# Kernel optimization log

Measured on AMD Instinct MI355X. Metric: run time of the kernel, lower is better.

## Reference

```python
import jax, jax.numpy as jnp
import numpy as np

D_MODEL = 1024
D_FFN = 4096
H = 16
D_HEAD = D_MODEL // H
B, L = 2, 2048
EPS = 1e-6


def layer_norm(x, a, b):
    # Matches torch: std is unbiased (ddof=1), and divides by (std + eps)
    mean = jnp.mean(x, axis=-1, keepdims=True)
    var = jnp.sum((x - mean) ** 2, axis=-1, keepdims=True) / (x.shape[-1] - 1)
    std = jnp.sqrt(var)
    return (x - mean) / (std + EPS) * a + b


def setup_inputs() -> dict:
    key = jax.random.key(0)
    ks = jax.random.split(key, 10)
    s = 0.02
    x = jax.random.normal(ks[0], (B, L, D_MODEL), dtype=jnp.float32)
    mask = jnp.tril(jnp.ones((L, L), dtype=jnp.int32))[None, None]  # causal [1,1,L,L]
    return {
        "x": x,
        "mask": mask,
        "Wqkv": jax.random.normal(ks[1], (D_MODEL, 3 * D_MODEL), jnp.float32) * s,
        "bqkv": jnp.zeros((3 * D_MODEL,), jnp.float32),
        "Wo": jax.random.normal(ks[2], (D_MODEL, D_MODEL), jnp.float32) * s,
        "bo": jnp.zeros((D_MODEL,), jnp.float32),
        "W1": jax.random.normal(ks[3], (D_MODEL, D_FFN), jnp.float32) * s,
        "b1": jnp.zeros((D_FFN,), jnp.float32),
        "W2": jax.random.normal(ks[4], (D_FFN, D_MODEL), jnp.float32) * s,
        "b2": jnp.zeros((D_MODEL,), jnp.float32),
        "ln1_a": jnp.ones((D_MODEL,), jnp.float32),
        "ln1_b": jnp.zeros((D_MODEL,), jnp.float32),
        "ln2_a": jnp.ones((D_MODEL,), jnp.float32),
        "ln2_b": jnp.zeros((D_MODEL,), jnp.float32),
    }


def reference(x, mask, Wqkv, bqkv, Wo, bo, W1, b1, W2, b2, ln1_a, ln1_b, ln2_a, ln2_b):
    b, l, d = x.shape
    # --- attention sublayer ---
    qkv = x @ Wqkv + bqkv                                   # [b, l, 3*d]
    qkv = qkv.reshape(b, l, 3, H, D_HEAD)                   # '(three h d)' ordering
    q, k, v = qkv[:, :, 0], qkv[:, :, 1], qkv[:, :, 2]      # each [b, l, h, dh]
    scores = jnp.einsum('bqhd,bkhd->bhqk', q, k) / jnp.sqrt(
        jnp.asarray(D_HEAD, x.dtype))                        # [b, h, lq, lk]
    scores = jnp.where(mask == 0, -jnp.inf, scores)
    p = jax.nn.softmax(scores, axis=-1)
    attn = jnp.einsum('bhqk,bkhd->bqhd', p, v).reshape(b, l, d)
    attn_out = attn @ Wo + bo
    x = layer_norm(x + attn_out, ln1_a, ln1_b)
    # --- MLP sublayer ---
    h = jax.nn.relu(x @ W1 + b1)
    mlp_out = h @ W2 + b2
    return layer_norm(x + mlp_out, ln2_a, ln2_b)
```

## Files before the change

### kernel.cpp

```cpp
#include <hip/hip_runtime.h>

#define D_MODEL 1024
#define D_FFN   4096
#define NH      16
#define DH      64
#define BB      2
#define LL      2048
#define MROWS   (BB * LL)

typedef unsigned short u16;
typedef unsigned int   u32;
typedef short bf16x8 __attribute__((ext_vector_type(8)));
typedef float f32x4  __attribute__((ext_vector_type(4)));

__device__ __forceinline__ float bf2f(u16 u) {
    union { u32 i; float f; } v;
    v.i = ((u32)u) << 16;
    return v.f;
}
__device__ __forceinline__ u16 f2bf(float f) {
    union { float f; u32 i; } v;
    v.f = f;
    u32 x = v.i;
    x += 0x7fffu + ((x >> 16) & 1u);
    return (u16)(x >> 16);
}
__device__ __forceinline__ float wave_sum(float v) {
    #pragma unroll
    for (int o = 32; o > 0; o >>= 1) v += __shfl_xor(v, o, 64);
    return v;
}
__device__ __forceinline__ u32 pack_bf_trunc(float a, float b) {
    return __builtin_amdgcn_perm(__float_as_uint(b), __float_as_uint(a),
                                 0x07060302u);
}

typedef const __attribute__((address_space(1))) u32 gu32;
typedef __attribute__((address_space(3))) u32 lu32;
__device__ __forceinline__ void gload_lds16(const void* g, void* l) {
    __builtin_amdgcn_global_load_lds((gu32*)g, (lu32*)l, 16, 0, 0);
}

__global__ __launch_bounds__(256) void cvt_kernel(
    const float* __restrict__ in, u16* __restrict__ out, int n)
{
    int i = (blockIdx.x * 256 + threadIdx.x) * 8;
    if (i >= n) return;
    float4 a = *(const float4*)(in + i);
    float4 b = *(const float4*)(in + i + 4);
    u16 o[8] = {f2bf(a.x), f2bf(a.y), f2bf(a.z), f2bf(a.w),
                f2bf(b.x), f2bf(b.y), f2bf(b.z), f2bf(b.w)};
    *(uint4*)(out + i) = *(const uint4*)o;
}

__global__ __launch_bounds__(256) void wt_kernel(
    const float* __restrict__ W, u16* __restrict__ Wt, int K, int N)
{
    __shared__ float tile[64][65];
    const int tid = threadIdx.x;
    const int n0 = blockIdx.x * 64;
    const int k0 = blockIdx.y * 64;

    int kr = tid >> 4;
    int nc = (tid & 15) * 4;
    #pragma unroll
    for (int p = 0; p < 4; ++p) {
        float4 v = *(const float4*)&W[(size_t)(k0 + kr + p * 16) * N + n0 + nc];
        tile[kr + p * 16][nc + 0] = v.x;
        tile[kr + p * 16][nc + 1] = v.y;
        tile[kr + p * 16][nc + 2] = v.z;
        tile[kr + p * 16][nc + 3] = v.w;
    }
    __syncthreads();

    int nr = tid >> 2;
    int kc = (tid & 3) * 16;
    u16 o[16];
    #pragma unroll
    for (int j = 0; j < 16; ++j) o[j] = f2bf(tile[kc + j][nr]);
    u16* dst = &Wt[(size_t)(n0 + nr) * K + k0 + kc];
    *(uint4*)dst       = *(const uint4*)&o[0];
    *(uint4*)(dst + 8) = *(const uint4*)&o[8];
}

template <int EPI, int RF32, int OF32>
__global__ __launch_bounds__(256) void gemm_bt_kernel(
    const u16* __restrict__ A, const u16* __restrict__ Bt,
    const float* __restrict__ bias, const void* __restrict__ resv,
    void* __restrict__ out0v, u16* __restrict__ out1, u16* __restrict__ out2,
    int M, int N, int K)
{
    __shared__ u16 sA[128 * 64];
    __shared__ u16 sB[128 * 64];

    const int tid  = threadIdx.x;
    const int lane = tid & 63;
    const int wave = tid >> 6;
    const int wm   = (wave & 1) * 64;
    const int wn   = (wave >> 1) * 64;
    const int quad = lane >> 4;
    const int l16  = lane & 15;

    const int nb  = gridDim.x;
    const int mb  = gridDim.y;
    const int f   = blockIdx.y * nb + blockIdx.x;
    const int xcd = f & 7;
    const int idx = f >> 3;
    const int rn  = nb >> 1;
    const int rm  = mb >> 2;
    const int n0  = ((xcd & 1) * rn + (idx % rn)) * 128;
    const int m0  = ((xcd >> 1) * rm + (idx / rn)) * 128;

    f32x4 acc[4][4];
    #pragma unroll
    for (int i = 0; i < 4; ++i)
        #pragma unroll
        for (int j = 0; j < 4; ++j)
            acc[i][j] = (f32x4){0.f, 0.f, 0.f, 0.f};

    const u16* Ablk = A  + (size_t)m0 * K;
    const u16* Bblk = Bt + (size_t)n0 * K;

    for (int k0 = 0; k0 < K; k0 += 64) {
        #pragma unroll
        for (int i = 0; i < 4; ++i) {
            int chunk = (i * 4 + wave) * 64 + lane;
            int r = chunk >> 3;
            int c = (chunk & 7) ^ (r & 7);
            size_t goff = (size_t)r * K + k0 + c * 8;
            gload_lds16(Ablk + goff, &sA[(i * 4 + wave) * 512]);
            gload_lds16(Bblk + goff, &sB[(i * 4 + wave) * 512]);
        }
        __syncthreads();

        #pragma unroll
        for (int ks = 0; ks < 2; ++ks) {
            bf16x8 af[4], bfr[4];
            #pragma unroll
            for (int i = 0; i < 4; ++i) {
                int R = wm + i * 16 + l16;
                int slot = R * 8 + ((ks * 4 + quad) ^ (R & 7));
                af[i] = *(const bf16x8*)&sA[slot * 8];
            }
            #pragma unroll
            for (int j = 0; j < 4; ++j) {
                int R = wn + j * 16 + l16;
                int slot = R * 8 + ((ks * 4 + quad) ^ (R & 7));
                bfr[j] = *(const bf16x8*)&sB[slot * 8];
            }
            #pragma unroll
            for (int i = 0; i < 4; ++i)
                #pragma unroll
                for (int j = 0; j < 4; ++j)
                    acc[i][j] = __builtin_amdgcn_mfma_f32_16x16x32_bf16(
                        af[i], bfr[j], acc[i][j], 0, 0, 0);
        }
        __syncthreads();
    }

    #pragma unroll
    for (int i = 0; i < 4; ++i) {
        int rowb = m0 + wm + i * 16 + quad * 4;
        #pragma unroll
        for (int j = 0; j < 4; ++j) {
            int col = n0 + wn + j * 16 + l16;
            float bv = bias[col];
            #pragma unroll
            for (int r = 0; r < 4; ++r) {
                int rr = rowb + r;
                float v = acc[i][j][r] + bv;
                if (EPI == 0) {
                    int which = col >> 10;
                    int h     = (col >> 6) & 15;
                    int d     = col & 63;
                    int b     = rr >> 11;
                    int l     = rr & 2047;
                    size_t idx2 = ((size_t)(b * NH + h) * LL + l) * DH + d;
                    u16* o0 = (u16*)out0v;
                    if (which == 0)      o0[idx2]   = f2bf(v * 0.125f);
                    else if (which == 1) out1[idx2] = f2bf(v);
                    else                 out2[idx2] = f2bf(v);
                } else {
                    size_t idx2 = (size_t)rr * N + col;
                    if (EPI == 1) {
                        v += RF32 ? ((const float*)resv)[idx2]
                                  : bf2f(((const u16*)resv)[idx2]);
                    } else {
                        v = v > 0.f ? v : 0.f;
                    }
                    if (OF32) ((float*)out0v)[idx2] = v;
                    else      ((u16*)out0v)[idx2]   = f2bf(v);
                }
            }
        }
    }
}

__global__ __launch_bounds__(256) void attn_kernel(
    const u16* __restrict__ Q, const u16* __restrict__ K,
    const u16* __restrict__ V, u16* __restrict__ out)
{
    __shared__ u16 ks[64 * 72];
    __shared__ u16 vs[64 * 72];
    __shared__ u16 ps[4][16 * 72];

    const int tid  = threadIdx.x;
    const int lane = tid & 63;
    const int wave = tid >> 6;
    const int l16  = lane & 15;
    const int quad = lane >> 4;

    const int f   = blockIdx.x;
    const int xcd = f & 7;
    const int idx = f >> 3;
    const int bh  = xcd * 4 + (idx >> 4);
    const int pr  = idx & 15;
    const int b   = bh >> 4, h = bh & 15;
    const size_t head_off = (size_t)bh * LL * DH;

    const u16* Qh = Q + head_off;
    const u16* Kh = K + head_off;
    const u16* Vh = V + head_off;

    const int qtA = 31 - pr, qtB = pr;
    const int baseA = qtA * 64 + wave * 16;
    const int baseB = qtB * 64 + wave * 16;
    const int qgA   = baseA + l16;
    const int qgB   = baseB + l16;

    const bf16x8 qfA0 = *(const bf16x8*)&Qh[(size_t)qgA * DH + quad * 8];
    const bf16x8 qfA1 = *(const bf16x8*)&Qh[(size_t)qgA * DH + 32 + quad * 8];
    const bf16x8 qfB0 = *(const bf16x8*)&Qh[(size_t)qgB * DH + quad * 8];
    const bf16x8 qfB1 = *(const bf16x8*)&Qh[(size_t)qgB * DH + 32 + quad * 8];

    float lA = 0.f, lB = 0.f;
    f32x4 oA[4], oB[4];
    #pragma unroll
    for (int t = 0; t < 4; ++t) {
        oA[t] = (f32x4){0.f, 0.f, 0.f, 0.f};
        oB[t] = (f32x4){0.f, 0.f, 0.f, 0.f};
    }

    u16* psw = &ps[wave][0];

    for (int c = 0; c <= qtA; ++c) {
        const bool doB = (c <= qtB);
        __syncthreads();
        {
            int key  = tid >> 2;
            int dim0 = (tid & 3) * 16;
            const u16* src = Kh + (size_t)(c * 64 + key) * DH + dim0;
            *(uint4*)&ks[key * 72 + dim0]     = *(const uint4*)src;
            *(uint4*)&ks[key * 72 + dim0 + 8] = *(const uint4*)(src + 8);
        }
        {
            int kp   = tid >> 3;
            int dim0 = (tid & 7) * 8;
            const u16* src = Vh + (size_t)(c * 64 + 2 * kp) * DH + dim0;
            uint4 v0 = *(const uint4*)src;
            uint4 v1 = *(const uint4*)(src + DH);
            const u32* w0 = (const u32*)&v0;
            const u32* w1 = (const u32*)&v1;
            #pragma unroll
            for (int e = 0; e < 8; ++e) {
                int d = dim0 + e;
                u32 lo = (w0[e >> 1] >> ((e & 1) * 16)) & 0xffffu;
                u32 hi = (w1[e >> 1] >> ((e & 1) * 16)) & 0xffffu;
                int csw = kp ^ (4 * ((d >> 3) & 7));
                *(u32*)&vs[d * 72 + 2 * csw] = lo | (hi << 16);
            }
        }
        __syncthreads();

        f32x4 stA[4], stB[4];
        #pragma unroll
        for (int t = 0; t < 4; ++t) {
            bf16x8 k0 = *(const bf16x8*)&ks[(t * 16 + l16) * 72 + quad * 8];
            bf16x8 k1 = *(const bf16x8*)&ks[(t * 16 + l16) * 72 + 32 + quad * 8];
            f32x4 s = (f32x4){0.f, 0.f, 0.f, 0.f};
            s = __builtin_amdgcn_mfma_f32_16x16x32_bf16(k0, qfA0, s, 0, 0, 0);
            s = __builtin_amdgcn_mfma_f32_16x16x32_bf16(k1, qfA1, s, 0, 0, 0);
            stA[t] = s;
            if (doB) {
                f32x4 s2 = (f32x4){0.f, 0.f, 0.f, 0.f};
                s2 = __builtin_amdgcn_mfma_f32_16x16x32_bf16(k0, qfB0, s2, 0, 0, 0);
                s2 = __builtin_amdgcn_mfma_f32_16x16x32_bf16(k1, qfB1, s2, 0, 0, 0);
                stB[t] = s2;
            }
        }

        if (c == qtA) {
            #pragma unroll
            for (int t = 0; t < 4; ++t)
                #pragma unroll
                for (int r = 0; r < 4; ++r)
                    if (c * 64 + t * 16 + quad * 4 + r > qgA) stA[t][r] = -INFINITY;
        }
        if (doB && c == qtB) {
            #pragma unroll
            for (int t = 0; t < 4; ++t)
                #pragma unroll
                for (int r = 0; r < 4; ++r)
                    if (c * 64 + t * 16 + quad * 4 + r > qgB) stB[t][r] = -INFINITY;
        }

        {
            float psum = 0.f;
            u32 pk[8];
            #pragma unroll
            for (int t = 0; t < 4; ++t) {
                float p0 = __expf(stA[t][0]), p1 = __expf(stA[t][1]);
                float p2 = __expf(stA[t][2]), p3 = __expf(stA[t][3]);
                psum += (p0 + p1) + (p2 + p3);
                pk[2 * t]     = pack_bf_trunc(p0, p1);
                pk[2 * t + 1] = pack_bf_trunc(p2, p3);
            }
            psum += __shfl_xor(psum, 16, 64);
            psum += __shfl_xor(psum, 32, 64);
            lA += psum;
            #pragma unroll
            for (int t = 0; t < 4; ++t) {
                uint2 w = {pk[2 * t], pk[2 * t + 1]};
                *(uint2*)&psw[l16 * 72 + t * 16 + quad * 4] = w;
            }
            bf16x8 pf0 = *(const bf16x8*)&psw[l16 * 72 + quad * 8];
            bf16x8 pf1 = *(const bf16x8*)&psw[l16 * 72 + 32 + quad * 8];
            #pragma unroll
            for (int dt = 0; dt < 4; ++dt) {
                int d  = dt * 16 + l16;
                int sw = 4 * ((d >> 3) & 7);
                bf16x8 vf0 = *(const bf16x8*)&vs[d * 72 + 2 * ((quad * 4) ^ sw)];
                bf16x8 vf1 = *(const bf16x8*)&vs[d * 72 + 2 * ((16 + quad * 4) ^ sw)];
                oA[dt] = __builtin_amdgcn_mfma_f32_16x16x32_bf16(pf0, vf0, oA[dt], 0, 0, 0);
                oA[dt] = __builtin_amdgcn_mfma_f32_16x16x32_bf16(pf1, vf1, oA[dt], 0, 0, 0);
            }
        }
        if (doB) {
            float psum = 0.f;
            u32 pk[8];
            #pragma unroll
            for (int t = 0; t < 4; ++t) {
                float p0 = __expf(stB[t][0]), p1 = __expf(stB[t][1]);
                float p2 = __expf(stB[t][2]), p3 = __expf(stB[t][3]);
                psum += (p0 + p1) + (p2 + p3);
                pk[2 * t]     = pack_bf_trunc(p0, p1);
                pk[2 * t + 1] = pack_bf_trunc(p2, p3);
            }
            psum += __shfl_xor(psum, 16, 64);
            psum += __shfl_xor(psum, 32, 64);
            lB += psum;
            #pragma unroll
            for (int t = 0; t < 4; ++t) {
                uint2 w = {pk[2 * t], pk[2 * t + 1]};
                *(uint2*)&psw[l16 * 72 + t * 16 + quad * 4] = w;
            }
            bf16x8 pf0 = *(const bf16x8*)&psw[l16 * 72 + quad * 8];
            bf16x8 pf1 = *(const bf16x8*)&psw[l16 * 72 + 32 + quad * 8];
            #pragma unroll
            for (int dt = 0; dt < 4; ++dt) {
                int d  = dt * 16 + l16;
                int sw = 4 * ((d >> 3) & 7);
                bf16x8 vf0 = *(const bf16x8*)&vs[d * 72 + 2 * ((quad * 4) ^ sw)];
                bf16x8 vf1 = *(const bf16x8*)&vs[d * 72 + 2 * ((16 + quad * 4) ^ sw)];
                oB[dt] = __builtin_amdgcn_mfma_f32_16x16x32_bf16(pf0, vf0, oB[dt], 0, 0, 0);
                oB[dt] = __builtin_amdgcn_mfma_f32_16x16x32_bf16(pf1, vf1, oB[dt], 0, 0, 0);
            }
        }
    }

    {
        float i0 = 1.f / __shfl(lA, quad * 4 + 0, 64);
        float i1 = 1.f / __shfl(lA, quad * 4 + 1, 64);
        float i2 = 1.f / __shfl(lA, quad * 4 + 2, 64);
        float i3 = 1.f / __shfl(lA, quad * 4 + 3, 64);
        #pragma unroll
        for (int dt = 0; dt < 4; ++dt) {
            size_t col = h * DH + dt * 16 + l16;
            size_t r0  = ((size_t)b * LL + baseA + quad * 4) * D_MODEL + col;
            out[r0]               = f2bf(oA[dt][0] * i0);
            out[r0 + D_MODEL]     = f2bf(oA[dt][1] * i1);
            out[r0 + 2 * D_MODEL] = f2bf(oA[dt][2] * i2);
            out[r0 + 3 * D_MODEL] = f2bf(oA[dt][3] * i3);
        }
    }
    {
        float i0 = 1.f / __shfl(lB, quad * 4 + 0, 64);
        float i1 = 1.f / __shfl(lB, quad * 4 + 1, 64);
        float i2 = 1.f / __shfl(lB, quad * 4 + 2, 64);
        float i3 = 1.f / __shfl(lB, quad * 4 + 3, 64);
        #pragma unroll
        for (int dt = 0; dt < 4; ++dt) {
            size_t col = h * DH + dt * 16 + l16;
            size_t r0  = ((size_t)b * LL + baseB + quad * 4) * D_MODEL + col;
            out[r0]               = f2bf(oB[dt][0] * i0);
            out[r0 + D_MODEL]     = f2bf(oB[dt][1] * i1);
            out[r0 + 2 * D_MODEL] = f2bf(oB[dt][2] * i2);
            out[r0 + 3 * D_MODEL] = f2bf(oB[dt][3] * i3);
        }
    }
}

template <int OF32>
__global__ __launch_bounds__(256) void ln_kernel(
    const float* __restrict__ t, const float* __restrict__ ga,
    const float* __restrict__ gb, void* __restrict__ outv)
{
    __shared__ float red[8];
    const int tid  = threadIdx.x;
    const int lane = tid & 63;
    const int wave = tid >> 6;
    const size_t row = blockIdx.x;

    const float* tr = t + row * D_MODEL;
    float4 u = *(const float4*)(tr + tid * 4);
    float x0 = u.x, x1 = u.y, x2 = u.z, x3 = u.w;

    float s = wave_sum(x0 + x1 + x2 + x3);
    if (lane == 0) red[wave] = s;
    __syncthreads();
    float mean = (red[0] + red[1] + red[2] + red[3]) * (1.f / 1024.f);

    float d0 = x0 - mean, d1 = x1 - mean, d2 = x2 - mean, d3 = x3 - mean;
    float v = wave_sum(d0 * d0 + d1 * d1 + d2 * d2 + d3 * d3);
    if (lane == 0) red[4 + wave] = v;
    __syncthreads();
    float var = (red[4] + red[5] + red[6] + red[7]) * (1.f / 1023.f);
    float inv = 1.f / (sqrtf(var) + 1e-6f);

    int c = tid * 4;
    float y0 = d0 * inv * ga[c + 0] + gb[c + 0];
    float y1 = d1 * inv * ga[c + 1] + gb[c + 1];
    float y2 = d2 * inv * ga[c + 2] + gb[c + 2];
    float y3 = d3 * inv * ga[c + 3] + gb[c + 3];
    if (OF32) {
        float4 y = {y0, y1, y2, y3};
        *(float4*)((float*)outv + row * D_MODEL + c) = y;
    } else {
        ushort4 y = {f2bf(y0), f2bf(y1), f2bf(y2), f2bf(y3)};
        *(ushort4*)((u16*)outv + row * D_MODEL + c) = y;
    }
}

extern "C" void kernel_launch(void* const* d_in, const int* in_sizes, int n_in,
                              void* d_out, int out_size, void* d_ws, size_t ws_size,
                              hipStream_t stream)
{
    const float* x    = (const float*)d_in[0];
    const float* Wqkv = (const float*)d_in[2];
    const float* bqkv = (const float*)d_in[3];
    const float* Wo   = (const float*)d_in[4];
    const float* bo   = (const float*)d_in[5];
    const float* W1   = (const float*)d_in[6];
    const float* b1   = (const float*)d_in[7];
    const float* W2   = (const float*)d_in[8];
    const float* b2   = (const float*)d_in[9];
    const float* ln1a = (const float*)d_in[10];
    const float* ln1b = (const float*)d_in[11];
    const float* ln2a = (const float*)d_in[12];
    const float* ln2b = (const float*)d_in[13];

    char* ws = (char*)d_ws;
    const size_t HSZ = (size_t)BB * NH * LL * DH;
    const size_t RSZ = (size_t)MROWS * D_MODEL;
    u16*   Qp    = (u16*)ws;
    u16*   Kp    = Qp + HSZ;
    u16*   Vp    = Kp + HSZ;
    u16*   attn  = Vp + HSZ;
    u16*   hbuf  = (u16*)ws;
    float* t1    = (float*)(ws + 33554432);
    u16*   xb    = (u16*)t1;
    u16*   x1    = (u16*)(ws + 50331648);
    u16*   Wqkvt = (u16*)(ws + 58720256);
    u16*   Wot   = (u16*)(ws + 65011712);
    u16*   W1t   = (u16*)(ws + 67108864);
    u16*   W2t   = (u16*)(ws + 75497472);
    float* t2    = t1;

    dim3 blk(256);

    cvt_kernel<<<dim3(RSZ / 2048), blk, 0, stream>>>(x, xb, (int)RSZ);
    wt_kernel<<<dim3(48, 16), blk, 0, stream>>>(Wqkv, Wqkvt, D_MODEL, 3 * D_MODEL);
    wt_kernel<<<dim3(16, 16), blk, 0, stream>>>(Wo,   Wot,   D_MODEL, D_MODEL);
    wt_kernel<<<dim3(64, 16), blk, 0, stream>>>(W1,   W1t,   D_MODEL, D_FFN);
    wt_kernel<<<dim3(16, 64), blk, 0, stream>>>(W2,   W2t,   D_FFN,   D_MODEL);

    gemm_bt_kernel<0,0,0><<<dim3(24, 32), blk, 0, stream>>>(
        xb, Wqkvt, bqkv, nullptr, Qp, Kp, Vp, MROWS, 3 * D_MODEL, D_MODEL);
    attn_kernel<<<dim3(512), blk, 0, stream>>>(Qp, Kp, Vp, attn);
    gemm_bt_kernel<1,1,1><<<dim3(8, 32), blk, 0, stream>>>(
        attn, Wot, bo, x, t1, nullptr, nullptr, MROWS, D_MODEL, D_MODEL);
    ln_kernel<0><<<dim3(MROWS), blk, 0, stream>>>(t1, ln1a, ln1b, x1);
    gemm_bt_kernel<2,0,0><<<dim3(32, 32), blk, 0, stream>>>(
        x1, W1t, b1, nullptr, hbuf, nullptr, nullptr, MROWS, D_FFN, D_MODEL);
    gemm_bt_kernel<1,0,1><<<dim3(8, 32), blk, 0, stream>>>(
        hbuf, W2t, b2, x1, t2, nullptr, nullptr, MROWS, D_MODEL, D_FFN);
    ln_kernel<1><<<dim3(MROWS), blk, 0, stream>>>(t2, ln2a, ln2b, d_out);
}
```

Baseline: 378.6 us.

## Split-K the W2 GEMM four ways with bf16 partials and a reduce kernel

```diff
diff --git a/kernel.cpp b/kernel.cpp
--- a/kernel.cpp
+++ b/kernel.cpp
@@ -83,7 +83,7 @@
     *(uint4*)(dst + 8) = *(const uint4*)&o[8];
 }
 
-template <int EPI, int RF32, int OF32>
+template <int EPI, int RF32, int OF32, int KS>
 __global__ __launch_bounds__(256) void gemm_bt_kernel(
     const u16* __restrict__ A, const u16* __restrict__ Bt,
     const float* __restrict__ bias, const void* __restrict__ resv,
@@ -109,7 +109,19 @@
     const int rn  = nb >> 1;
     const int rm  = mb >> 2;
     const int n0  = ((xcd & 1) * rn + (idx % rn)) * 128;
-    const int m0  = ((xcd >> 1) * rm + (idx / rn)) * 128;
+    const int ym  = (xcd >> 1) * rm + (idx / rn);
+
+    int s, m0;
+    if (KS > 1) {
+        const int mt = mb / KS;
+        s  = ym / mt;
+        m0 = (ym % mt) * 128;
+    } else {
+        s  = 0;
+        m0 = ym * 128;
+    }
+    const int Kseg = K / KS;
+    const int kbeg = s * Kseg;
 
     f32x4 acc[4][4];
     #pragma unroll
@@ -121,7 +133,7 @@
     const u16* Ablk = A  + (size_t)m0 * K;
     const u16* Bblk = Bt + (size_t)n0 * K;
 
-    for (int k0 = 0; k0 < K; k0 += 64) {
+    for (int k0 = kbeg; k0 < kbeg + Kseg; k0 += 64) {
         #pragma unroll
         for (int i = 0; i < 4; ++i) {
             int chunk = (i * 4 + wave) * 64 + lane;
@@ -164,7 +176,7 @@
         #pragma unroll
         for (int j = 0; j < 4; ++j) {
             int col = n0 + wn + j * 16 + l16;
-            float bv = bias[col];
+            float bv = (EPI == 3) ? 0.f : bias[col];
             #pragma unroll
             for (int r = 0; r < 4; ++r) {
                 int rr = rowb + r;
@@ -180,6 +192,8 @@
                     if (which == 0)      o0[idx2]   = f2bf(v * 0.125f);
                     else if (which == 1) out1[idx2] = f2bf(v);
                     else                 out2[idx2] = f2bf(v);
+                } else if (EPI == 3) {
+                    ((u16*)out0v)[((size_t)s * M + rr) * N + col] = f2bf(v);
                 } else {
                     size_t idx2 = (size_t)rr * N + col;
                     if (EPI == 1) {
@@ -194,6 +208,42 @@
             }
         }
     }
+}
+
+__global__ __launch_bounds__(256) void reduce4_kernel(
+    const u16* __restrict__ P, const float* __restrict__ bias,
+    const u16* __restrict__ res, float* __restrict__ out)
+{
+    const size_t SL = (size_t)MROWS * D_MODEL;
+    size_t i = ((size_t)blockIdx.x * 256 + threadIdx.x) * 8;
+    int col = (int)(i & (D_MODEL - 1));
+
+    uint4 p0 = *(const uint4*)(P + i);
+    uint4 p1 = *(const uint4*)(P + SL + i);
+    uint4 p2 = *(const uint4*)(P + 2 * SL + i);
+    uint4 p3 = *(const uint4*)(P + 3 * SL + i);
+    uint4 rr = *(const uint4*)(res + i);
+    float4 b0 = *(const float4*)(bias + col);
+    float4 b1 = *(const float4*)(bias + col + 4);
+
+    const u32* w0 = (const u32*)&p0;
+    const u32* w1 = (const u32*)&p1;
+    const u32* w2 = (const u32*)&p2;
+    const u32* w3 = (const u32*)&p3;
+    const u32* wr = (const u32*)&rr;
+    float o[8];
+    #pragma unroll
+    for (int e = 0; e < 8; ++e) {
+        int dw = e >> 1, sh = (e & 1) * 16;
+        float v = bf2f((u16)(w0[dw] >> sh)) + bf2f((u16)(w1[dw] >> sh))
+                + bf2f((u16)(w2[dw] >> sh)) + bf2f((u16)(w3[dw] >> sh))
+                + bf2f((u16)(wr[dw] >> sh));
+        o[e] = v;
+    }
+    o[0] += b0.x; o[1] += b0.y; o[2] += b0.z; o[3] += b0.w;
+    o[4] += b1.x; o[5] += b1.y; o[6] += b1.z; o[7] += b1.w;
+    *(float4*)(out + i)     = (float4){o[0], o[1], o[2], o[3]};
+    *(float4*)(out + i + 4) = (float4){o[4], o[5], o[6], o[7]};
 }
 
 __global__ __launch_bounds__(256) void attn_kernel(
@@ -474,6 +524,7 @@
     u16*   Wot   = (u16*)(ws + 65011712);
     u16*   W1t   = (u16*)(ws + 67108864);
     u16*   W2t   = (u16*)(ws + 75497472);
+    u16*   Pbuf  = (u16*)(ws + 83886080);
     float* t2    = t1;
 
     dim3 blk(256);
@@ -484,15 +535,16 @@
     wt_kernel<<<dim3(64, 16), blk, 0, stream>>>(W1,   W1t,   D_MODEL, D_FFN);
     wt_kernel<<<dim3(16, 64), blk, 0, stream>>>(W2,   W2t,   D_FFN,   D_MODEL);
 
-    gemm_bt_kernel<0,0,0><<<dim3(24, 32), blk, 0, stream>>>(
+    gemm_bt_kernel<0,0,0,1><<<dim3(24, 32), blk, 0, stream>>>(
         xb, Wqkvt, bqkv, nullptr, Qp, Kp, Vp, MROWS, 3 * D_MODEL, D_MODEL);
     attn_kernel<<<dim3(512), blk, 0, stream>>>(Qp, Kp, Vp, attn);
-    gemm_bt_kernel<1,1,1><<<dim3(8, 32), blk, 0, stream>>>(
+    gemm_bt_kernel<1,1,1,1><<<dim3(8, 32), blk, 0, stream>>>(
         attn, Wot, bo, x, t1, nullptr, nullptr, MROWS, D_MODEL, D_MODEL);
     ln_kernel<0><<<dim3(MROWS), blk, 0, stream>>>(t1, ln1a, ln1b, x1);
-    gemm_bt_kernel<2,0,0><<<dim3(32, 32), blk, 0, stream>>>(
+    gemm_bt_kernel<2,0,0,1><<<dim3(32, 32), blk, 0, stream>>>(
         x1, W1t, b1, nullptr, hbuf, nullptr, nullptr, MROWS, D_FFN, D_MODEL);
-    gemm_bt_kernel<1,0,1><<<dim3(8, 32), blk, 0, stream>>>(
-        hbuf, W2t, b2, x1, t2, nullptr, nullptr, MROWS, D_MODEL, D_FFN);
+    gemm_bt_kernel<3,0,0,4><<<dim3(8, 128), blk, 0, stream>>>(
+        hbuf, W2t, b2, nullptr, Pbuf, nullptr, nullptr, MROWS, D_MODEL, D_FFN);
+    reduce4_kernel<<<dim3(RSZ / 2048), blk, 0, stream>>>(Pbuf, b2, x1, t2);
     ln_kernel<1><<<dim3(MROWS), blk, 0, stream>>>(t2, ln2a, ln2b, d_out);
 }
```

New measurement: 366.2 us. 1.03x faster.
